# Kernel optimization log

Measured on AMD Instinct MI355X. Metric: run time of the kernel, lower is better.

## Reference

```python
import jax, jax.numpy as jnp
import numpy as np

N = 100000   # nodes
E = 1600000  # edges
H = 128      # hidden / feature dim
G = 64       # graphs in batch
L = 3        # GCN layers
EPS = 1e-5


def setup_inputs() -> dict:
    key = jax.random.key(0)
    ks = jax.random.split(key, 8)
    return {
        "x": jax.random.normal(ks[0], (N, H), jnp.float32),
        "edge_index": jax.random.randint(ks[1], (2, E), 0, N, dtype=jnp.int64),
        "batch": jnp.sort(jax.random.randint(ks[2], (N,), 0, G, dtype=jnp.int64)),
        "conv_w": jax.random.normal(ks[3], (L, H, H), jnp.float32) * 0.05,
        "conv_b": jnp.zeros((L, H), jnp.float32),
        "bn_g": jnp.ones((L, H), jnp.float32),
        "bn_b": jnp.zeros((L, H), jnp.float32),
        "attn_w1": jax.random.normal(ks[4], (H, H), jnp.float32) * 0.05,
        "attn_b1": jnp.zeros((H,), jnp.float32),
        "attn_w2": jax.random.normal(ks[5], (H, 1), jnp.float32) * 0.05,
        "attn_b2": jnp.zeros((1,), jnp.float32),
        "proj_w1": jax.random.normal(ks[6], (H, H), jnp.float32) * 0.05,
        "proj_b1": jnp.zeros((H,), jnp.float32),
        "proj_w2": jax.random.normal(ks[7], (H, H), jnp.float32) * 0.05,
        "proj_b2": jnp.zeros((H,), jnp.float32),
    }


def reference(x, edge_index, batch, conv_w, conv_b, bn_g, bn_b,
              attn_w1, attn_b1, attn_w2, attn_b2,
              proj_w1, proj_b1, proj_w2, proj_b2):
    n = x.shape[0]
    # GCNConv normalization: add self-loops, norm = d^-1/2[src] * d^-1/2[dst]
    loops = jnp.arange(n)
    src = jnp.concatenate([edge_index[0], loops])
    dst = jnp.concatenate([edge_index[1], loops])
    deg = jax.ops.segment_sum(jnp.ones_like(src, dtype=x.dtype), dst, num_segments=n)
    dinv = jax.lax.rsqrt(deg)  # deg >= 1 due to self-loops
    norm = (dinv[src] * dinv[dst])[:, None]  # [E+N, 1]

    h = x
    for i in range(L):
        identity = h
        z = h @ conv_w[i]                                          # [N, H]
        agg = jax.ops.segment_sum(z[src] * norm, dst, num_segments=n) + conv_b[i]
        # BatchNorm1d (training: batch statistics, biased variance)
        mean = jnp.mean(agg, axis=0)
        var = jnp.mean(jnp.square(agg - mean), axis=0)
        z = (agg - mean) * jax.lax.rsqrt(var + EPS) * bn_g[i] + bn_b[i]
        z = jax.nn.relu(z)
        if i > 0:
            z = z + identity
        h = z

    # Graph attention: softmax over all nodes (dim=0), elementwise reweight
    a = jnp.tanh(h @ attn_w1 + attn_b1) @ attn_w2 + attn_b2        # [N, 1]
    a = jax.nn.softmax(a, axis=0)
    h = h * a

    # global_mean_pool over batch ids
    sums = jax.ops.segment_sum(h, batch, num_segments=G)           # [G, H]
    counts = jax.ops.segment_sum(jnp.ones((n, 1), x.dtype), batch, num_segments=G)
    pooled = sums / jnp.maximum(counts, 1.0)

    # projection MLP
    out = jax.nn.relu(pooled @ proj_w1 + proj_b1) @ proj_w2 + proj_b2
    return out
```

## Files before the change

### kernel.cpp

```cpp
#include <hip/hip_runtime.h>

#define HH 128
#define GG 64
#define EPS 1e-5f

__device__ __forceinline__ unsigned femax_enc(float f) {
    unsigned u = __float_as_uint(f);
    return (u & 0x80000000u) ? ~u : (u | 0x80000000u);
}
__device__ __forceinline__ float femax_dec(unsigned u) {
    return (u & 0x80000000u) ? __uint_as_float(u & 0x7FFFFFFFu) : __uint_as_float(~u);
}

__global__ void k_count(const int* __restrict__ dst, int* __restrict__ cnt, int E) {
    int i = blockIdx.x * blockDim.x + threadIdx.x;
    if (i < E) atomicAdd(&cnt[dst[i]], 1);
}

__global__ __launch_bounds__(512) void k_scanA(const int* __restrict__ cnt, int* __restrict__ tmp,
                                               int* __restrict__ bsum, int n) {
    __shared__ int s[512];
    int t = threadIdx.x;
    int i = blockIdx.x * 512 + t;
    s[t] = (i < n) ? cnt[i] : 0;
    __syncthreads();
    for (int o = 1; o < 512; o <<= 1) {
        int u = (t >= o) ? s[t - o] : 0;
        __syncthreads();
        s[t] += u;
        __syncthreads();
    }
    if (i < n) tmp[i] = s[t];
    if (t == 511) bsum[blockIdx.x] = s[511];
}

__global__ __launch_bounds__(512) void k_scanB(int* __restrict__ bsum, int nb) {
    __shared__ int s[512];
    int t = threadIdx.x;
    s[t] = (t < nb) ? bsum[t] : 0;
    __syncthreads();
    for (int o = 1; o < 512; o <<= 1) {
        int u = (t >= o) ? s[t - o] : 0;
        __syncthreads();
        s[t] += u;
        __syncthreads();
    }
    if (t < nb) bsum[t] = s[t];
}

__global__ void k_scanC(const int* __restrict__ tmp, const int* __restrict__ bsum,
                        const int* __restrict__ cnt, int* __restrict__ rowptr,
                        float* __restrict__ dinv, int n) {
    int i = blockIdx.x * blockDim.x + threadIdx.x;
    if (i < n) {
        int b = i >> 9;
        int off = (b > 0) ? bsum[b - 1] : 0;
        rowptr[i + 1] = tmp[i] + off;
        if (i == 0) rowptr[0] = 0;
        dinv[i] = rsqrtf((float)(cnt[i] + 1));
    }
}

__global__ void k_fill(const int* __restrict__ src, const int* __restrict__ dst,
                       const int* __restrict__ rowptr, int* __restrict__ cursor,
                       const float* __restrict__ dinv, int2* __restrict__ epk, int E) {
    int e = blockIdx.x * blockDim.x + threadIdx.x;
    if (e < E) {
        int s0 = src[e], d0 = dst[e];
        int p = atomicAdd(&cursor[d0], 1);
        int idx = rowptr[d0] + p;
        epk[idx] = make_int2(s0, __float_as_int(dinv[s0] * dinv[d0]));
    }
}

#define FMA_ROW(i, a)                       \
    acc[i][0] = fmaf(a, w0.x, acc[i][0]);   \
    acc[i][1] = fmaf(a, w0.y, acc[i][1]);   \
    acc[i][2] = fmaf(a, w0.z, acc[i][2]);   \
    acc[i][3] = fmaf(a, w0.w, acc[i][3]);   \
    acc[i][4] = fmaf(a, w1.x, acc[i][4]);   \
    acc[i][5] = fmaf(a, w1.y, acc[i][5]);   \
    acc[i][6] = fmaf(a, w1.z, acc[i][6]);   \
    acc[i][7] = fmaf(a, w1.w, acc[i][7]);

template <int ACT>
__global__ __launch_bounds__(256, 2) void k_gemm(const float* __restrict__ A, const float* __restrict__ W,
                                                 const float* __restrict__ bias, float* __restrict__ C,
                                                 const float* __restrict__ w2, const float* __restrict__ b2,
                                                 unsigned* __restrict__ gmax, int n) {
    __shared__ float hl[64][132];
    __shared__ float Ws[64][128];
    int tb = blockIdx.x * 64;
    int t = threadIdx.x;
    int rows = n - tb; if (rows > 64) rows = 64;
    for (int idx = t; idx < 64 * 32; idx += 256) {
        int r = idx >> 5, c4 = (idx & 31) << 2;
        if (r < rows)
            *(float4*)&hl[r][c4] = *(const float4*)&A[(size_t)(tb + r) * HH + c4];
    }
    int tx = t & 15;
    int ty = t >> 4;
    int tx8 = tx << 3;
    float acc[4][8] = {};
    for (int kc = 0; kc < 2; ++kc) {
        __syncthreads();
        for (int idx = t; idx < 64 * 32; idx += 256) {
            int r = idx >> 5, c4 = (idx & 31) << 2;
            *(float4*)&Ws[r][c4] = *(const float4*)&W[(size_t)(kc * 64 + r) * HH + c4];
        }
        __syncthreads();
        int kb = kc * 64;
        for (int k = 0; k < 64; ++k) {
            float4 w0 = *(const float4*)&Ws[k][tx8];
            float4 w1 = *(const float4*)&Ws[k][tx8 + 4];
            float a0 = hl[ty][kb + k];
            float a1 = hl[ty + 16][kb + k];
            float a2 = hl[ty + 32][kb + k];
            float a3 = hl[ty + 48][kb + k];
            FMA_ROW(0, a0)
            FMA_ROW(1, a1)
            FMA_ROW(2, a2)
            FMA_ROW(3, a3)
        }
    }
    if (ACT == 0) {
#pragma unroll
        for (int i = 0; i < 4; ++i) {
            int r = tb + ty + 16 * i;
            if (r < n) {
                float4 o0 = {acc[i][0], acc[i][1], acc[i][2], acc[i][3]};
                float4 o1 = {acc[i][4], acc[i][5], acc[i][6], acc[i][7]};
                *(float4*)&C[(size_t)r * HH + tx8] = o0;
                *(float4*)&C[(size_t)r * HH + tx8 + 4] = o1;
            }
        }
    } else {
        float b1v[8], w2v[8];
#pragma unroll
        for (int j = 0; j < 8; ++j) { b1v[j] = bias[tx8 + j]; w2v[j] = w2[tx8 + j]; }
        float b2s = b2[0];
        float lmax = -3.4e38f;
#pragma unroll
        for (int i = 0; i < 4; ++i) {
            float s = 0.f;
#pragma unroll
            for (int j = 0; j < 8; ++j)
                s = fmaf(tanhf(acc[i][j] + b1v[j]), w2v[j], s);
            s += __shfl_xor(s, 1);
            s += __shfl_xor(s, 2);
            s += __shfl_xor(s, 4);
            s += __shfl_xor(s, 8);
            int r = tb + ty + 16 * i;
            float val = s + b2s;
            if (r < n) {
                lmax = fmaxf(lmax, val);
                if (tx == 0) C[r] = val;
            }
        }
        lmax = fmaxf(lmax, __shfl_xor(lmax, 16));
        lmax = fmaxf(lmax, __shfl_xor(lmax, 32));
        __shared__ float wm[4];
        if ((t & 63) == 0) wm[t >> 6] = lmax;
        __syncthreads();
        if (t == 0) {
            float m = fmaxf(fmaxf(wm[0], wm[1]), fmaxf(wm[2], wm[3]));
            atomicMax(gmax, femax_enc(m));
        }
    }
}

#define AGG_FMA(vv, ww)                                           \
    acc.x = fmaf(vv.x, ww, acc.x); acc.y = fmaf(vv.y, ww, acc.y); \
    acc.z = fmaf(vv.z, ww, acc.z); acc.w = fmaf(vv.w, ww, acc.w);

__global__ __launch_bounds__(256) void k_agg(const float* __restrict__ z, const int* __restrict__ rowptr,
                                             const int2* __restrict__ epk, const float* __restrict__ dinv,
                                             const float* __restrict__ bias, float* __restrict__ agg, int n) {
    int wid = (int)((blockIdx.x * (size_t)blockDim.x + threadIdx.x) >> 6);
    if (wid >= n) return;
    int lane = threadIdx.x & 63;
    int half = lane >> 5;
    int c0 = (lane & 31) << 2;
    int beg = rowptr[wid], end = rowptr[wid + 1];
    float4 acc = {0.f, 0.f, 0.f, 0.f};
    if (half == 0) {
        float di = dinv[wid];
        float ws = di * di;
        float4 zs = *(const float4*)&z[(size_t)wid * HH + c0];
        acc.x = zs.x * ws; acc.y = zs.y * ws; acc.z = zs.z * ws; acc.w = zs.w * ws;
    }
    for (int e = beg + half; e < end; e += 16) {
        int2 p[8];
        float w[8];
#pragma unroll
        for (int j = 0; j < 8; ++j) {
            int idx = e + 2 * j;
            bool valid = idx < end;
            p[j] = epk[valid ? idx : beg];
            w[j] = valid ? __int_as_float(p[j].y) : 0.f;
        }
        float4 v[8];
#pragma unroll
        for (int j = 0; j < 8; ++j)
            v[j] = *(const float4*)&z[(size_t)p[j].x * HH + c0];
#pragma unroll
        for (int j = 0; j < 8; ++j) { AGG_FMA(v[j], w[j]) }
    }
    acc.x += __shfl_xor(acc.x, 32);
    acc.y += __shfl_xor(acc.y, 32);
    acc.z += __shfl_xor(acc.z, 32);
    acc.w += __shfl_xor(acc.w, 32);
    if (half == 0) {
        float4 b4 = *(const float4*)&bias[c0];
        acc.x += b4.x; acc.y += b4.y; acc.z += b4.z; acc.w += b4.w;
        *(float4*)&agg[(size_t)wid * HH + c0] = acc;
    }
}

__global__ __launch_bounds__(256) void k_bnstats(const float* __restrict__ agg, float* __restrict__ colsum,
                                                 float* __restrict__ colsq, int n) {
    int t = threadIdx.x;
    int col = t & 127, sub = t >> 7;
    int rpb = (n + gridDim.x - 1) / gridDim.x;
    int r0 = blockIdx.x * rpb;
    int r1 = r0 + rpb; if (r1 > n) r1 = n;
    float s = 0.f, q = 0.f;
    for (int r = r0 + sub; r < r1; r += 2) {
        float v = agg[(size_t)r * HH + col];
        s += v;
        q = fmaf(v, v, q);
    }
    __shared__ float ls[256], lq[256];
    ls[t] = s; lq[t] = q;
    __syncthreads();
    if (t < 128) {
        atomicAdd(&colsum[col], ls[t] + ls[t + 128]);
        atomicAdd(&colsq[col], lq[t] + lq[t + 128]);
    }
}

__global__ void k_bnapply(const float* __restrict__ agg, const float* __restrict__ colsum,
                          const float* __restrict__ colsq, const float* __restrict__ g,
                          const float* __restrict__ b, const float* __restrict__ hin,
                          float* __restrict__ hout, int n, int residual) {
    int i = blockIdx.x * blockDim.x + threadIdx.x;
    int nvec4 = n * (HH / 4);
    if (i >= nvec4) return;
    int c = (i << 2) & 127;
    float4 cs = *(const float4*)&colsum[c];
    float4 cq = *(const float4*)&colsq[c];
    float4 gg = *(const float4*)&g[c];
    float4 bb = *(const float4*)&b[c];
    float inv_n = 1.0f / (float)n;
    float m0 = cs.x * inv_n, m1 = cs.y * inv_n, m2 = cs.z * inv_n, m3 = cs.w * inv_n;
    float A0 = rsqrtf(cq.x * inv_n - m0 * m0 + EPS) * gg.x;
    float A1 = rsqrtf(cq.y * inv_n - m1 * m1 + EPS) * gg.y;
    float A2 = rsqrtf(cq.z * inv_n - m2 * m2 + EPS) * gg.z;
    float A3 = rsqrtf(cq.w * inv_n - m3 * m3 + EPS) * gg.w;
    float B0 = bb.x - m0 * A0, B1 = bb.y - m1 * A1, B2 = bb.z - m2 * A2, B3 = bb.w - m3 * A3;
    float4 v = *(const float4*)&agg[(size_t)i * 4];
    v.x = fmaxf(fmaf(v.x, A0, B0), 0.f);
    v.y = fmaxf(fmaf(v.y, A1, B1), 0.f);
    v.z = fmaxf(fmaf(v.z, A2, B2), 0.f);
    v.w = fmaxf(fmaf(v.w, A3, B3), 0.f);
    if (residual) {
        float4 h0 = *(const float4*)&hin[(size_t)i * 4];
        v.x += h0.x; v.y += h0.y; v.z += h0.z; v.w += h0.w;
    }
    *(float4*)&hout[(size_t)i * 4] = v;
}

__global__ __launch_bounds__(256) void k_redsum(const float* __restrict__ a, const unsigned* __restrict__ gmax,
                                                float* __restrict__ psum, int n) {
    float M = femax_dec(*gmax);
    float acc = 0.f;
    for (int i = blockIdx.x * blockDim.x + threadIdx.x; i < n; i += gridDim.x * blockDim.x)
        acc += expf(a[i] - M);
    __shared__ float s[256];
    s[threadIdx.x] = acc;
    __syncthreads();
    for (int o = 128; o > 0; o >>= 1) {
        if (threadIdx.x < o) s[threadIdx.x] += s[threadIdx.x + o];
        __syncthreads();
    }
    if (threadIdx.x == 0) psum[blockIdx.x] = s[0];
}

__global__ __launch_bounds__(256) void k_pool(const float* __restrict__ h, const float* __restrict__ apre,
                                              const int* __restrict__ batch, const unsigned* __restrict__ gmax,
                                              float* __restrict__ pooled, float* __restrict__ counts, int n) {
    float M = femax_dec(*gmax);
    int t = threadIdx.x;
    int col = t & 127, sub = t >> 7;
    int rpb = (n + gridDim.x - 1) / gridDim.x;
    int r0 = blockIdx.x * rpb;
    int r1 = r0 + rpb; if (r1 > n) r1 = n;
    float acc = 0.f, cntf = 0.f;
    int cur = -1;
    for (int r = r0 + sub; r < r1; r += 2) {
        int g = batch[r];
        if (g != cur) {
            if (cur >= 0) {
                atomicAdd(&pooled[cur * HH + col], acc);
                if (col == 0) atomicAdd(&counts[cur], cntf);
            }
            cur = g; acc = 0.f; cntf = 0.f;
        }
        float s = expf(apre[r] - M);
        acc = fmaf(h[(size_t)r * HH + col], s, acc);
        cntf += 1.0f;
    }
    if (cur >= 0) {
        atomicAdd(&pooled[cur * HH + col], acc);
        if (col == 0) atomicAdd(&counts[cur], cntf);
    }
}

__global__ __launch_bounds__(128) void k_mlp(const float* __restrict__ pooled, const float* __restrict__ counts,
                                             const float* __restrict__ psum, const float* __restrict__ W1,
                                             const float* __restrict__ b1, const float* __restrict__ W2,
                                             const float* __restrict__ b2, float* __restrict__ out) {
    int g = blockIdx.x;
    int t = threadIdx.x;
    __shared__ float ss[128];
    __shared__ float p[128], t1[128];
    ss[t] = psum[t] + psum[t + 128];
    __syncthreads();
    for (int o = 64; o > 0; o >>= 1) {
        if (t < o) ss[t] += ss[t + o];
        __syncthreads();
    }
    float S = ss[0];
    float c = fmaxf(counts[g], 1.0f);
    p[t] = pooled[g * HH + t] / (S * c);
    __syncthreads();
    float acc = b1[t];
    for (int k = 0; k < 128; ++k) acc = fmaf(p[k], W1[k * HH + t], acc);
    t1[t] = fmaxf(acc, 0.f);
    __syncthreads();
    float acc2 = b2[t];
    for (int j = 0; j < 128; ++j) acc2 = fmaf(t1[j], W2[j * HH + t], acc2);
    out[g * HH + t] = acc2;
}

extern "C" void kernel_launch(void* const* d_in, const int* in_sizes, int n_in,
                              void* d_out, int out_size, void* d_ws, size_t ws_size,
                              hipStream_t stream) {
    const float* x       = (const float*)d_in[0];
    const int*   ei      = (const int*)d_in[1];
    const int*   batch   = (const int*)d_in[2];
    const float* conv_w  = (const float*)d_in[3];
    const float* conv_b  = (const float*)d_in[4];
    const float* bn_g    = (const float*)d_in[5];
    const float* bn_b    = (const float*)d_in[6];
    const float* attn_w1 = (const float*)d_in[7];
    const float* attn_b1 = (const float*)d_in[8];
    const float* attn_w2 = (const float*)d_in[9];
    const float* attn_b2 = (const float*)d_in[10];
    const float* proj_w1 = (const float*)d_in[11];
    const float* proj_b1 = (const float*)d_in[12];
    const float* proj_w2 = (const float*)d_in[13];
    const float* proj_b2 = (const float*)d_in[14];

    const int E = in_sizes[1] / 2;
    const int n = in_sizes[2];
    const int* srcp = ei;
    const int* dstp = ei + E;

    char* base = (char*)d_ws;
    size_t off = 0;
    auto alloc = [&](size_t bytes) -> char* {
        char* p = base + off;
        off = (off + bytes + 511) & ~(size_t)511;
        return p;
    };
    int*   cntcur  = (int*)alloc((size_t)2 * n * 4);
    int*   cnt     = cntcur;
    int*   cursor  = cntcur + n;
    int*   rowptr  = (int*)alloc((size_t)(n + 1) * 4);
    int*   tmp     = (int*)alloc((size_t)n * 4);
    int*   bsum    = (int*)alloc(512 * 4);
    float* dinv    = (float*)alloc((size_t)n * 4);
    int2*  epk     = (int2*)alloc((size_t)E * 8);
    float* h       = (float*)alloc((size_t)n * HH * 4);
    float* z       = (float*)alloc((size_t)n * HH * 4);
    float* agg     = (float*)alloc((size_t)n * HH * 4);
    float* colsum  = (float*)alloc(512);
    float* colsq   = (float*)alloc(512);
    float* apre    = (float*)alloc((size_t)n * 4);
    unsigned* gmaxu = (unsigned*)alloc(512);
    float* psum    = (float*)alloc(1024);
    float* pooled  = (float*)alloc(GG * HH * 4 + 512);
    float* counts  = pooled + GG * HH;

    const int eGrid    = (E + 255) / 256;
    const int nGrid    = (n + 255) / 256;
    const int nbScan   = (n + 511) / 512;
    const int gemmGrid = (n + 63) / 64;
    const int waveGrid = (n + 3) / 4;
    const int bnGrid   = (n * (HH / 4) + 255) / 256;

    hipMemsetAsync(cntcur, 0, (size_t)2 * n * 4, stream);
    k_count<<<eGrid, 256, 0, stream>>>(dstp, cnt, E);
    k_scanA<<<nbScan, 512, 0, stream>>>(cnt, tmp, bsum, n);
    k_scanB<<<1, 512, 0, stream>>>(bsum, nbScan);
    k_scanC<<<nGrid, 256, 0, stream>>>(tmp, bsum, cnt, rowptr, dinv, n);
    k_fill<<<eGrid, 256, 0, stream>>>(srcp, dstp, rowptr, cursor, dinv, epk, E);

    for (int l = 0; l < 3; ++l) {
        const float* A = (l == 0) ? x : h;
        k_gemm<0><<<gemmGrid, 256, 0, stream>>>(A, conv_w + (size_t)l * HH * HH, nullptr, z,
                                                nullptr, nullptr, nullptr, n);
        k_agg<<<waveGrid, 256, 0, stream>>>(z, rowptr, epk, dinv, conv_b + l * HH, agg, n);
        hipMemsetAsync(colsum, 0, 1024, stream);
        k_bnstats<<<1024, 256, 0, stream>>>(agg, colsum, colsq, n);
        k_bnapply<<<bnGrid, 256, 0, stream>>>(agg, colsum, colsq, bn_g + l * HH, bn_b + l * HH,
                                              h, h, n, (l > 0) ? 1 : 0);
    }

    hipMemsetAsync(gmaxu, 0, 4, stream);
    k_gemm<1><<<gemmGrid, 256, 0, stream>>>(h, attn_w1, attn_b1, apre, attn_w2, attn_b2, gmaxu, n);
    k_redsum<<<256, 256, 0, stream>>>(apre, gmaxu, psum, n);

    hipMemsetAsync(pooled, 0, GG * HH * 4 + 512, stream);
    k_pool<<<1024, 256, 0, stream>>>(h, apre, batch, gmaxu, pooled, counts, n);
    k_mlp<<<GG, 128, 0, stream>>>(pooled, counts, psum, proj_w1, proj_b1, proj_w2, proj_b2,
                                  (float*)d_out);
}
```

Baseline: 1.121 ms.

## Fuse BatchNorm apply and residual into next GEMM prologue; fold softmax sum into pool

Removes the standalone BN-apply kernel by applying normalization, ReLU and the residual add while loading the A tile in the following GEMM, which also writes the activated tensor back in place for later residual use. Drops the separate softmax-denominator reduction by accumulating the exp sum inside the pooling kernel with one atomic per block. Consolidates the small memsets into a single arena memset, halves the W tile in shared memory and raises launch bounds to 3 blocks per CU. This saves full N×H read/write passes and several launches, at the cost of extra global writes from the GEMM and more atomics on a single float.

```diff
diff --git a/kernel.cpp b/kernel.cpp
--- a/kernel.cpp
+++ b/kernel.cpp
@@ -83,34 +83,69 @@
     acc[i][6] = fmaf(a, w1.z, acc[i][6]);   \
     acc[i][7] = fmaf(a, w1.w, acc[i][7]);
 
-template <int ACT>
-__global__ __launch_bounds__(256, 2) void k_gemm(const float* __restrict__ A, const float* __restrict__ W,
-                                                 const float* __restrict__ bias, float* __restrict__ C,
-                                                 const float* __restrict__ w2, const float* __restrict__ b2,
-                                                 unsigned* __restrict__ gmax, int n) {
+template <int BNIN, int ACT>
+__global__ __launch_bounds__(256, 3) void k_gemm(const float* __restrict__ Ain, float* __restrict__ Aio,
+                                                 const float* __restrict__ res,
+                                                 const float* __restrict__ csum, const float* __restrict__ csq,
+                                                 const float* __restrict__ bng, const float* __restrict__ bnb,
+                                                 const float* __restrict__ W, const float* __restrict__ bias,
+                                                 float* __restrict__ C, const float* __restrict__ w2,
+                                                 const float* __restrict__ b2, unsigned* __restrict__ gmax,
+                                                 int n) {
     __shared__ float hl[64][132];
-    __shared__ float Ws[64][128];
+    __shared__ float Ws[32][128];
     int tb = blockIdx.x * 64;
     int t = threadIdx.x;
     int rows = n - tb; if (rows > 64) rows = 64;
+    int c4 = (t & 31) << 2;
+
+    float A0c = 0.f, A1c = 0.f, A2c = 0.f, A3c = 0.f;
+    float B0c = 0.f, B1c = 0.f, B2c = 0.f, B3c = 0.f;
+    if (BNIN) {
+        float4 cs = *(const float4*)&csum[c4];
+        float4 cq = *(const float4*)&csq[c4];
+        float4 gg = *(const float4*)&bng[c4];
+        float4 bb = *(const float4*)&bnb[c4];
+        float inv_n = 1.0f / (float)n;
+        float m0 = cs.x * inv_n, m1 = cs.y * inv_n, m2 = cs.z * inv_n, m3 = cs.w * inv_n;
+        A0c = rsqrtf(cq.x * inv_n - m0 * m0 + EPS) * gg.x;
+        A1c = rsqrtf(cq.y * inv_n - m1 * m1 + EPS) * gg.y;
+        A2c = rsqrtf(cq.z * inv_n - m2 * m2 + EPS) * gg.z;
+        A3c = rsqrtf(cq.w * inv_n - m3 * m3 + EPS) * gg.w;
+        B0c = bb.x - m0 * A0c; B1c = bb.y - m1 * A1c; B2c = bb.z - m2 * A2c; B3c = bb.w - m3 * A3c;
+    }
     for (int idx = t; idx < 64 * 32; idx += 256) {
-        int r = idx >> 5, c4 = (idx & 31) << 2;
-        if (r < rows)
-            *(float4*)&hl[r][c4] = *(const float4*)&A[(size_t)(tb + r) * HH + c4];
+        int r = idx >> 5;
+        if (r < rows) {
+            size_t go = (size_t)(tb + r) * HH + c4;
+            float4 v = *(const float4*)&Ain[go];
+            if (BNIN) {
+                v.x = fmaxf(fmaf(v.x, A0c, B0c), 0.f);
+                v.y = fmaxf(fmaf(v.y, A1c, B1c), 0.f);
+                v.z = fmaxf(fmaf(v.z, A2c, B2c), 0.f);
+                v.w = fmaxf(fmaf(v.w, A3c, B3c), 0.f);
+                if (res) {
+                    float4 rv = *(const float4*)&res[go];
+                    v.x += rv.x; v.y += rv.y; v.z += rv.z; v.w += rv.w;
+                }
+                *(float4*)&Aio[go] = v;
+            }
+            *(float4*)&hl[r][c4] = v;
+        }
     }
     int tx = t & 15;
     int ty = t >> 4;
     int tx8 = tx << 3;
     float acc[4][8] = {};
-    for (int kc = 0; kc < 2; ++kc) {
-        __syncthreads();
-        for (int idx = t; idx < 64 * 32; idx += 256) {
-            int r = idx >> 5, c4 = (idx & 31) << 2;
-            *(float4*)&Ws[r][c4] = *(const float4*)&W[(size_t)(kc * 64 + r) * HH + c4];
-        }
-        __syncthreads();
-        int kb = kc * 64;
-        for (int k = 0; k < 64; ++k) {
+    for (int kc = 0; kc < 4; ++kc) {
+        __syncthreads();
+        for (int idx = t; idx < 32 * 32; idx += 256) {
+            int r = idx >> 5, cc4 = (idx & 31) << 2;
+            *(float4*)&Ws[r][cc4] = *(const float4*)&W[(size_t)(kc * 32 + r) * HH + cc4];
+        }
+        __syncthreads();
+        int kb = kc * 32;
+        for (int k = 0; k < 32; ++k) {
             float4 w0 = *(const float4*)&Ws[k][tx8];
             float4 w1 = *(const float4*)&Ws[k][tx8 + 4];
             float a0 = hl[ty][kb + k];
@@ -239,63 +274,17 @@
     }
 }
 
-__global__ void k_bnapply(const float* __restrict__ agg, const float* __restrict__ colsum,
-                          const float* __restrict__ colsq, const float* __restrict__ g,
-                          const float* __restrict__ b, const float* __restrict__ hin,
-                          float* __restrict__ hout, int n, int residual) {
-    int i = blockIdx.x * blockDim.x + threadIdx.x;
-    int nvec4 = n * (HH / 4);
-    if (i >= nvec4) return;
-    int c = (i << 2) & 127;
-    float4 cs = *(const float4*)&colsum[c];
-    float4 cq = *(const float4*)&colsq[c];
-    float4 gg = *(const float4*)&g[c];
-    float4 bb = *(const float4*)&b[c];
-    float inv_n = 1.0f / (float)n;
-    float m0 = cs.x * inv_n, m1 = cs.y * inv_n, m2 = cs.z * inv_n, m3 = cs.w * inv_n;
-    float A0 = rsqrtf(cq.x * inv_n - m0 * m0 + EPS) * gg.x;
-    float A1 = rsqrtf(cq.y * inv_n - m1 * m1 + EPS) * gg.y;
-    float A2 = rsqrtf(cq.z * inv_n - m2 * m2 + EPS) * gg.z;
-    float A3 = rsqrtf(cq.w * inv_n - m3 * m3 + EPS) * gg.w;
-    float B0 = bb.x - m0 * A0, B1 = bb.y - m1 * A1, B2 = bb.z - m2 * A2, B3 = bb.w - m3 * A3;
-    float4 v = *(const float4*)&agg[(size_t)i * 4];
-    v.x = fmaxf(fmaf(v.x, A0, B0), 0.f);
-    v.y = fmaxf(fmaf(v.y, A1, B1), 0.f);
-    v.z = fmaxf(fmaf(v.z, A2, B2), 0.f);
-    v.w = fmaxf(fmaf(v.w, A3, B3), 0.f);
-    if (residual) {
-        float4 h0 = *(const float4*)&hin[(size_t)i * 4];
-        v.x += h0.x; v.y += h0.y; v.z += h0.z; v.w += h0.w;
-    }
-    *(float4*)&hout[(size_t)i * 4] = v;
-}
-
-__global__ __launch_bounds__(256) void k_redsum(const float* __restrict__ a, const unsigned* __restrict__ gmax,
-                                                float* __restrict__ psum, int n) {
-    float M = femax_dec(*gmax);
-    float acc = 0.f;
-    for (int i = blockIdx.x * blockDim.x + threadIdx.x; i < n; i += gridDim.x * blockDim.x)
-        acc += expf(a[i] - M);
-    __shared__ float s[256];
-    s[threadIdx.x] = acc;
-    __syncthreads();
-    for (int o = 128; o > 0; o >>= 1) {
-        if (threadIdx.x < o) s[threadIdx.x] += s[threadIdx.x + o];
-        __syncthreads();
-    }
-    if (threadIdx.x == 0) psum[blockIdx.x] = s[0];
-}
-
 __global__ __launch_bounds__(256) void k_pool(const float* __restrict__ h, const float* __restrict__ apre,
                                               const int* __restrict__ batch, const unsigned* __restrict__ gmax,
-                                              float* __restrict__ pooled, float* __restrict__ counts, int n) {
+                                              float* __restrict__ pooled, float* __restrict__ counts,
+                                              float* __restrict__ Sglob, int n) {
     float M = femax_dec(*gmax);
     int t = threadIdx.x;
     int col = t & 127, sub = t >> 7;
     int rpb = (n + gridDim.x - 1) / gridDim.x;
     int r0 = blockIdx.x * rpb;
     int r1 = r0 + rpb; if (r1 > n) r1 = n;
-    float acc = 0.f, cntf = 0.f;
+    float acc = 0.f, cntf = 0.f, es = 0.f;
     int cur = -1;
     for (int r = r0 + sub; r < r1; r += 2) {
         int g = batch[r];
@@ -309,28 +298,23 @@
         float s = expf(apre[r] - M);
         acc = fmaf(h[(size_t)r * HH + col], s, acc);
         cntf += 1.0f;
+        if (col == 0) es += s;
     }
     if (cur >= 0) {
         atomicAdd(&pooled[cur * HH + col], acc);
         if (col == 0) atomicAdd(&counts[cur], cntf);
     }
+    if (col == 0 && es != 0.f) atomicAdd(Sglob, es);
 }
 
 __global__ __launch_bounds__(128) void k_mlp(const float* __restrict__ pooled, const float* __restrict__ counts,
-                                             const float* __restrict__ psum, const float* __restrict__ W1,
+                                             const float* __restrict__ Sglob, const float* __restrict__ W1,
                                              const float* __restrict__ b1, const float* __restrict__ W2,
                                              const float* __restrict__ b2, float* __restrict__ out) {
     int g = blockIdx.x;
     int t = threadIdx.x;
-    __shared__ float ss[128];
     __shared__ float p[128], t1[128];
-    ss[t] = psum[t] + psum[t + 128];
-    __syncthreads();
-    for (int o = 64; o > 0; o >>= 1) {
-        if (t < o) ss[t] += ss[t + o];
-        __syncthreads();
-    }
-    float S = ss[0];
+    float S = Sglob[0];
     float c = fmaxf(counts[g], 1.0f);
     p[t] = pooled[g * HH + t] / (S * c);
     __syncthreads();
@@ -382,24 +366,27 @@
     int*   bsum    = (int*)alloc(512 * 4);
     float* dinv    = (float*)alloc((size_t)n * 4);
     int2*  epk     = (int2*)alloc((size_t)E * 8);
-    float* h       = (float*)alloc((size_t)n * HH * 4);
     float* z       = (float*)alloc((size_t)n * HH * 4);
-    float* agg     = (float*)alloc((size_t)n * HH * 4);
-    float* colsum  = (float*)alloc(512);
-    float* colsq   = (float*)alloc(512);
+    float* aggA    = (float*)alloc((size_t)n * HH * 4);
+    float* aggB    = (float*)alloc((size_t)n * HH * 4);
     float* apre    = (float*)alloc((size_t)n * 4);
-    unsigned* gmaxu = (unsigned*)alloc(512);
-    float* psum    = (float*)alloc(1024);
-    float* pooled  = (float*)alloc(GG * HH * 4 + 512);
-    float* counts  = pooled + GG * HH;
+    float* zarena  = (float*)alloc((size_t)(1024 + GG * HH + GG) * 4);
+    float* cs0 = zarena;            float* cq0 = zarena + 128;
+    float* cs1 = zarena + 256;      float* cq1 = zarena + 384;
+    float* cs2 = zarena + 512;      float* cq2 = zarena + 640;
+    unsigned* gmaxu = (unsigned*)(zarena + 768);
+    float* Sglob  = zarena + 769;
+    float* pooled = zarena + 1024;
+    float* counts = zarena + 1024 + GG * HH;
+    const size_t zbytes = (size_t)(1024 + GG * HH + GG) * 4;
 
     const int eGrid    = (E + 255) / 256;
     const int nGrid    = (n + 255) / 256;
     const int nbScan   = (n + 511) / 512;
     const int gemmGrid = (n + 63) / 64;
     const int waveGrid = (n + 3) / 4;
-    const int bnGrid   = (n * (HH / 4) + 255) / 256;
-
+
+    hipMemsetAsync(zarena, 0, zbytes, stream);
     hipMemsetAsync(cntcur, 0, (size_t)2 * n * 4, stream);
     k_count<<<eGrid, 256, 0, stream>>>(dstp, cnt, E);
     k_scanA<<<nbScan, 512, 0, stream>>>(cnt, tmp, bsum, n);
@@ -407,23 +394,27 @@
     k_scanC<<<nGrid, 256, 0, stream>>>(tmp, bsum, cnt, rowptr, dinv, n);
     k_fill<<<eGrid, 256, 0, stream>>>(srcp, dstp, rowptr, cursor, dinv, epk, E);
 
-    for (int l = 0; l < 3; ++l) {
-        const float* A = (l == 0) ? x : h;
-        k_gemm<0><<<gemmGrid, 256, 0, stream>>>(A, conv_w + (size_t)l * HH * HH, nullptr, z,
-                                                nullptr, nullptr, nullptr, n);
-        k_agg<<<waveGrid, 256, 0, stream>>>(z, rowptr, epk, dinv, conv_b + l * HH, agg, n);
-        hipMemsetAsync(colsum, 0, 1024, stream);
-        k_bnstats<<<1024, 256, 0, stream>>>(agg, colsum, colsq, n);
-        k_bnapply<<<bnGrid, 256, 0, stream>>>(agg, colsum, colsq, bn_g + l * HH, bn_b + l * HH,
-                                              h, h, n, (l > 0) ? 1 : 0);
-    }
-
-    hipMemsetAsync(gmaxu, 0, 4, stream);
-    k_gemm<1><<<gemmGrid, 256, 0, stream>>>(h, attn_w1, attn_b1, apre, attn_w2, attn_b2, gmaxu, n);
-    k_redsum<<<256, 256, 0, stream>>>(apre, gmaxu, psum, n);
-
-    hipMemsetAsync(pooled, 0, GG * HH * 4 + 512, stream);
-    k_pool<<<1024, 256, 0, stream>>>(h, apre, batch, gmaxu, pooled, counts, n);
-    k_mlp<<<GG, 128, 0, stream>>>(pooled, counts, psum, proj_w1, proj_b1, proj_w2, proj_b2,
+    k_gemm<0, 0><<<gemmGrid, 256, 0, stream>>>(x, nullptr, nullptr, nullptr, nullptr, nullptr, nullptr,
+                                               conv_w, nullptr, z, nullptr, nullptr, nullptr, n);
+    k_agg<<<waveGrid, 256, 0, stream>>>(z, rowptr, epk, dinv, conv_b, aggA, n);
+    k_bnstats<<<1024, 256, 0, stream>>>(aggA, cs0, cq0, n);
+
+    k_gemm<1, 0><<<gemmGrid, 256, 0, stream>>>(aggA, aggA, nullptr, cs0, cq0, bn_g, bn_b,
+                                               conv_w + (size_t)HH * HH, nullptr, z, nullptr, nullptr,
+                                               nullptr, n);
+    k_agg<<<waveGrid, 256, 0, stream>>>(z, rowptr, epk, dinv, conv_b + HH, aggB, n);
+    k_bnstats<<<1024, 256, 0, stream>>>(aggB, cs1, cq1, n);
+
+    k_gemm<1, 0><<<gemmGrid, 256, 0, stream>>>(aggB, aggB, aggA, cs1, cq1, bn_g + HH, bn_b + HH,
+                                               conv_w + (size_t)2 * HH * HH, nullptr, z, nullptr, nullptr,
+                                               nullptr, n);
+    k_agg<<<waveGrid, 256, 0, stream>>>(z, rowptr, epk, dinv, conv_b + 2 * HH, aggA, n);
+    k_bnstats<<<1024, 256, 0, stream>>>(aggA, cs2, cq2, n);
+
+    k_gemm<1, 1><<<gemmGrid, 256, 0, stream>>>(aggA, aggA, aggB, cs2, cq2, bn_g + 2 * HH, bn_b + 2 * HH,
+                                               attn_w1, attn_b1, apre, attn_w2, attn_b2, gmaxu, n);
+
+    k_pool<<<1024, 256, 0, stream>>>(aggA, apre, batch, gmaxu, pooled, counts, Sglob, n);
+    k_mlp<<<GG, 128, 0, stream>>>(pooled, counts, Sglob, proj_w1, proj_b1, proj_w2, proj_b2,
                                   (float*)d_out);
 }
```

Result: faster. 1.081 ms (-3.6%).
